# Kernel optimization log

Hardware: AMD Instinct MI355X
Metric: run time of the kernel (lower is better)

## Reference

```python
import jax, jax.numpy as jnp
import numpy as np


def setup_inputs() -> dict:
    key = jax.random.key(0)
    ks = jax.random.split(key, 16)
    B, S, L2 = 16, 1024, 2048

    def rn(k, shape, scale=0.1):
        return jax.random.normal(k, shape, dtype=jnp.float32) * scale

    return {
        "x": rn(ks[0], (B, S, 3), 1.0),
        "v1": rn(ks[1], (B, L2 + 1, 3), 1.0),
        "v2": rn(ks[2], (B, L2 + 1, 3), 1.0),
        # Attention: Linear(6, 1)
        "attn_w": rn(ks[3], (1, 6)),
        "attn_b": rn(ks[4], (1,)),
        # fc1: Linear(3, 16)
        "fc1_w": rn(ks[5], (16, 3)),
        "fc1_b": rn(ks[6], (16,)),
        # LSTM(16, 32, 1), gate order i,f,g,o -> 4*32 = 128
        "w_ih": rn(ks[7], (128, 16)),
        "w_hh": rn(ks[8], (128, 32)),
        "b_ih": rn(ks[9], (128,)),
        "b_hh": rn(ks[10], (128,)),
        # fc2: Linear(38, 16)
        "fc2_w": rn(ks[11], (16, 38)),
        "fc2_b": rn(ks[12], (16,)),
        # fc3: Linear(16, 3)
        "fc3_w": rn(ks[13], (3, 16)),
        "fc3_b": rn(ks[14], (3,)),
    }


def _attention(x, v, attn_w, attn_b):
    # Linear(6,1) over cat([x_i, key_j]) decomposes into x-part + key-part,
    # avoiding the original [B,S,L2,6] repeat/cat intermediate (same math).
    key_, value = v[:, :-1], v[:, 1:]          # [B,L2,3] each
    wx, wk = attn_w[0, :3], attn_w[0, 3:]
    scores = (x @ wx)[:, :, None] + (key_ @ wk)[:, None, :] + attn_b[0]  # [B,S,L2]
    a = jax.nn.softmax(scores, axis=-1)
    return jnp.einsum('bij,bjd->bid', a, value)  # [B,S,3]


def _lstm(x, w_ih, w_hh, b_ih, b_hh):
    # Single-layer batch_first LSTM, zero initial state, pytorch gate order i,f,g,o.
    B = x.shape[0]
    H = w_hh.shape[1]
    xg = x @ w_ih.T + (b_ih + b_hh)  # [B,S,4H] precomputed input contribution

    def step(carry, g_t):
        h, c = carry
        g = g_t + h @ w_hh.T
        i, f, gg, o = jnp.split(g, 4, axis=-1)
        c = jax.nn.sigmoid(f) * c + jax.nn.sigmoid(i) * jnp.tanh(gg)
        h = jax.nn.sigmoid(o) * jnp.tanh(c)
        return (h, c), h

    init = (jnp.zeros((B, H), x.dtype), jnp.zeros((B, H), x.dtype))
    _, hs = jax.lax.scan(step, init, jnp.swapaxes(xg, 0, 1))  # [S,B,H]
    return jnp.swapaxes(hs, 0, 1)  # [B,S,H]


def reference(x, v1, v2, attn_w, attn_b, fc1_w, fc1_b,
              w_ih, w_hh, b_ih, b_hh, fc2_w, fc2_b, fc3_w, fc3_b):
    a1 = _attention(x, v1, attn_w, attn_b)   # [B,S,3]
    a2 = _attention(x, v2, attn_w, attn_b)   # [B,S,3]
    h = _lstm(x @ fc1_w.T + fc1_b, w_ih, w_hh, b_ih, b_hh)  # [B,S,32]
    cat = jnp.concatenate([a1, a2, h], axis=-1)              # [B,S,38]
    out = jax.nn.relu(cat @ fc2_w.T + fc2_b) @ fc3_w.T + fc3_b
    return out  # [B,S,3]
```

## Files before the change

### kernel.cpp

```cpp
#include <hip/hip_runtime.h>
#include <hip/hip_bf16.h>

#define B_ 16
#define S_ 1024
#define L_ 2048
#define H_ 32

static __device__ __forceinline__ float sigm(float v) {
    return __builtin_amdgcn_rcpf(1.0f + __expf(-v));
}

static __device__ __forceinline__ float block_red_max(float v, float* buf, int tid) {
#pragma unroll
    for (int o = 32; o; o >>= 1) v = fmaxf(v, __shfl_down(v, o));
    if ((tid & 63) == 0) buf[tid >> 6] = v;
    __syncthreads();
    v = fmaxf(fmaxf(buf[0], buf[1]), fmaxf(buf[2], buf[3]));
    __syncthreads();
    return v;
}
static __device__ __forceinline__ float block_red_sum(float v, float* buf, int tid) {
#pragma unroll
    for (int o = 32; o; o >>= 1) v += __shfl_down(v, o);
    if ((tid & 63) == 0) buf[tid >> 6] = v;
    __syncthreads();
    v = buf[0] + buf[1] + buf[2] + buf[3];
    __syncthreads();
    return v;
}

__global__ __launch_bounds__(256) void attn_kernel(
    const float* __restrict__ v1, const float* __restrict__ v2,
    const float* __restrict__ attn_w, float* __restrict__ A)
{
    const int b   = blockIdx.x & 15;
    const int sel = blockIdx.x >> 4;
    const float* v = (sel ? v2 : v1) + (size_t)b * ((L_ + 1) * 3);
    const float wk0 = attn_w[3], wk1 = attn_w[4], wk2 = attn_w[5];
    const int tid = threadIdx.x;
    __shared__ float buf[4];

    float s[8];
    float mx = -3.4e38f;
#pragma unroll
    for (int k = 0; k < 8; ++k) {
        int jj = tid + (k << 8);
        const float* p = v + jj * 3;
        float sc = fmaf(p[2], wk2, fmaf(p[1], wk1, p[0] * wk0));
        s[k] = sc;
        mx = fmaxf(mx, sc);
    }
    mx = block_red_max(mx, buf, tid);

    float den = 0.f, a0 = 0.f, a1 = 0.f, a2 = 0.f;
#pragma unroll
    for (int k = 0; k < 8; ++k) {
        int jj = tid + (k << 8);
        float e = __expf(s[k] - mx);
        den += e;
        const float* p = v + (jj + 1) * 3;
        a0 = fmaf(e, p[0], a0);
        a1 = fmaf(e, p[1], a1);
        a2 = fmaf(e, p[2], a2);
    }
    den = block_red_sum(den, buf, tid);
    a0  = block_red_sum(a0,  buf, tid);
    a1  = block_red_sum(a1,  buf, tid);
    a2  = block_red_sum(a2,  buf, tid);
    if (tid == 0) {
        float inv = 1.0f / den;
        float* dst = A + sel * 48 + b * 3;
        dst[0] = a0 * inv; dst[1] = a1 * inv; dst[2] = a2 * inv;
    }
}

__global__ __launch_bounds__(64) void lstm_kernel(
    const float* __restrict__ x,
    const float* __restrict__ fc1_w,
    const float* __restrict__ fc1_b,
    const float* __restrict__ w_ih,
    const float* __restrict__ w_hh,
    const float* __restrict__ b_ih,
    const float* __restrict__ b_hh,
    float* __restrict__ h_out)
{
    const int b  = blockIdx.x;
    const int l  = threadIdx.x;
    const int j  = l & 31;
    const int hi = l >> 5;
    const int r0 = hi ? (32 + j) : j;
    const int r1 = hi ? (96 + j) : (64 + j);

    __shared__ float lds_x[S_ * 3];
    __shared__ float lds_h[64];

    {
        const float4* src = (const float4*)(x + (size_t)b * (S_ * 3));
        float4* dst = (float4*)lds_x;
#pragma unroll
        for (int m = 0; m < 12; ++m) dst[l + 64 * m] = src[l + 64 * m];
    }
    if (l < 32) lds_h[l] = 0.f;

    float wh0[H_], wh1[H_];
    {
        const float4* p0 = (const float4*)(w_hh + r0 * H_);
        const float4* p1 = (const float4*)(w_hh + r1 * H_);
#pragma unroll
        for (int m = 0; m < 8; ++m) {
            float4 a = p0[m];
            wh0[4*m] = a.x; wh0[4*m+1] = a.y; wh0[4*m+2] = a.z; wh0[4*m+3] = a.w;
            float4 c2 = p1[m];
            wh1[4*m] = c2.x; wh1[4*m+1] = c2.y; wh1[4*m+2] = c2.z; wh1[4*m+3] = c2.w;
        }
    }
    float W00 = 0, W01 = 0, W02 = 0, W10 = 0, W11 = 0, W12 = 0, bb0, bb1;
    {
        float s0 = 0, s1 = 0;
#pragma unroll
        for (int k = 0; k < 16; ++k) {
            float wi0 = w_ih[r0 * 16 + k], wi1 = w_ih[r1 * 16 + k];
            float f0 = fc1_w[k * 3 + 0], f1 = fc1_w[k * 3 + 1], f2 = fc1_w[k * 3 + 2];
            float fb = fc1_b[k];
            W00 = fmaf(wi0, f0, W00); W01 = fmaf(wi0, f1, W01); W02 = fmaf(wi0, f2, W02);
            s0  = fmaf(wi0, fb, s0);
            W10 = fmaf(wi1, f0, W10); W11 = fmaf(wi1, f1, W11); W12 = fmaf(wi1, f2, W12);
            s1  = fmaf(wi1, fb, s1);
        }
        bb0 = s0 + b_ih[r0] + b_hh[r0];
        bb1 = s1 + b_ih[r1] + b_hh[r1];
    }
    const float m1 = hi ? 1.0f : 2.0f;
    float c = 0.f;
    float* hob = h_out + ((size_t)b << 15);
    __syncthreads();

    for (int t = 0; t < S_; ++t) {
        const int rb = (t & 1) << 5;
        const int wb = rb ^ 32;
        float x0 = lds_x[3 * t], x1 = lds_x[3 * t + 1], x2 = lds_x[3 * t + 2];
        float a0 = fmaf(W02, x2, fmaf(W01, x1, fmaf(W00, x0, bb0)));
        float a1 = fmaf(W12, x2, fmaf(W11, x1, fmaf(W10, x0, bb1)));
#pragma unroll
        for (int m = 0; m < 8; ++m) {
            float4 hv = *(const float4*)&lds_h[rb + 4 * m];
            a0 = fmaf(wh0[4*m+0], hv.x, a0); a1 = fmaf(wh1[4*m+0], hv.x, a1);
            a0 = fmaf(wh0[4*m+1], hv.y, a0); a1 = fmaf(wh1[4*m+1], hv.y, a1);
            a0 = fmaf(wh0[4*m+2], hv.z, a0); a1 = fmaf(wh1[4*m+2], hv.z, a1);
            a0 = fmaf(wh0[4*m+3], hv.w, a0); a1 = fmaf(wh1[4*m+3], hv.w, a1);
        }
        float s0 = sigm(a0);
        float s1 = sigm(a1 * m1);
        float t0 = __shfl_xor(s0, 32);
        float t1 = __shfl_xor(s1, 32);
        float si = hi ? t0 : s0;
        float sf = hi ? s0 : t0;
        float sg = hi ? t1 : s1;
        float so = hi ? s1 : t1;
        float tg = fmaf(2.f, sg, -1.f);
        c = fmaf(sf, c, si * tg);
        float tc = fmaf(2.f, sigm(2.f * c), -1.f);
        float hval = so * tc;
        if (!hi) {
            lds_h[wb + j] = hval;
            hob[(t << 5) + j] = hval;
        }
        __syncthreads();
    }
}

__global__ __launch_bounds__(256) void final_kernel(
    const float* __restrict__ h,
    const float* __restrict__ A,
    const float* __restrict__ fc2_w,
    const float* __restrict__ fc2_b,
    const float* __restrict__ fc3_w,
    const float* __restrict__ fc3_b,
    float* __restrict__ out)
{
    __shared__ float sw2[16 * 38], sb2[16], sw3[48], sb3[3], sA[96];
    const int tid = threadIdx.x;
    for (int i = tid; i < 16 * 38; i += 256) sw2[i] = fc2_w[i];
    if (tid < 96) sA[tid] = A[tid];
    if (tid < 16) sb2[tid] = fc2_b[tid];
    if (tid < 48) sw3[tid] = fc3_w[tid];
    if (tid < 3)  sb3[tid] = fc3_b[tid];
    __syncthreads();

    const int p = blockIdx.x * 256 + tid;
    if (p >= B_ * S_) return;
    const int b = p >> 10;

    float hv[32];
    {
        const float4* hp = (const float4*)(h + ((size_t)p << 5));
#pragma unroll
        for (int m = 0; m < 8; ++m) {
            float4 t = hp[m];
            hv[4*m] = t.x; hv[4*m+1] = t.y; hv[4*m+2] = t.z; hv[4*m+3] = t.w;
        }
    }
    const float a10 = sA[b*3+0], a11 = sA[b*3+1], a12 = sA[b*3+2];
    const float a20 = sA[48+b*3+0], a21 = sA[48+b*3+1], a22 = sA[48+b*3+2];

    float y[16];
#pragma unroll
    for (int u = 0; u < 16; ++u) {
        const float* w = sw2 + u * 38;
        float acc = sb2[u];
        acc = fmaf(w[0], a10, acc); acc = fmaf(w[1], a11, acc); acc = fmaf(w[2], a12, acc);
        acc = fmaf(w[3], a20, acc); acc = fmaf(w[4], a21, acc); acc = fmaf(w[5], a22, acc);
#pragma unroll
        for (int k = 0; k < 32; ++k) acc = fmaf(w[6 + k], hv[k], acc);
        y[u] = fmaxf(acc, 0.f);
    }
#pragma unroll
    for (int d = 0; d < 3; ++d) {
        float o = sb3[d];
#pragma unroll
        for (int u = 0; u < 16; ++u) o = fmaf(sw3[d * 16 + u], y[u], o);
        out[p * 3 + d] = o;
    }
}

extern "C" void kernel_launch(void* const* d_in, const int* in_sizes, int n_in,
                              void* d_out, int out_size, void* d_ws, size_t ws_size,
                              hipStream_t stream) {
    const float* x      = (const float*)d_in[0];
    const float* v1     = (const float*)d_in[1];
    const float* v2     = (const float*)d_in[2];
    const float* attn_w = (const float*)d_in[3];
    const float* fc1_w  = (const float*)d_in[5];
    const float* fc1_b  = (const float*)d_in[6];
    const float* w_ih   = (const float*)d_in[7];
    const float* w_hh   = (const float*)d_in[8];
    const float* b_ih   = (const float*)d_in[9];
    const float* b_hh   = (const float*)d_in[10];
    const float* fc2_w  = (const float*)d_in[11];
    const float* fc2_b  = (const float*)d_in[12];
    const float* fc3_w  = (const float*)d_in[13];
    const float* fc3_b  = (const float*)d_in[14];
    float* out = (float*)d_out;

    float* Aws = (float*)d_ws;
    float* hws = (float*)((char*)d_ws + 4096);

    attn_kernel <<<32, 256, 0, stream>>>(v1, v2, attn_w, Aws);
    lstm_kernel <<<16, 64, 0, stream>>>(x, fc1_w, fc1_b, w_ih, w_hh, b_ih, b_hh, hws);
    final_kernel<<<64, 256, 0, stream>>>(hws, Aws, fc2_w, fc2_b, fc3_w, fc3_b, out);
}
```

Before: 432.7 us.

## Fuse attention into LSTM launch and streamline recurrent step without barriers

Merges the attention reduction into the LSTM kernel as 32 extra single-wave blocks using only wave shuffles, dropping one kernel launch. In the recurrent loop it removes the per-step __syncthreads, relying on the 64-thread block being a single wave64. It also splits the h vector dot product into two packed-FMA accumulator chains and uses exp2 with prescaled constants. Finally it unrolls by two with fixed double-buffer offsets and gives the global h store to the upper half-wave. The aim is a shorter serial latency per timestep. The cost is that correctness now depends on in-order LDS access within one wave, with no explicit barrier.

```diff
diff --git a/kernel.cpp b/kernel.cpp
--- a/kernel.cpp
+++ b/kernel.cpp
@@ -6,86 +6,76 @@
 #define L_ 2048
 #define H_ 32
 
-static __device__ __forceinline__ float sigm(float v) {
-    return __builtin_amdgcn_rcpf(1.0f + __expf(-v));
-}
-
-static __device__ __forceinline__ float block_red_max(float v, float* buf, int tid) {
-#pragma unroll
-    for (int o = 32; o; o >>= 1) v = fmaxf(v, __shfl_down(v, o));
-    if ((tid & 63) == 0) buf[tid >> 6] = v;
-    __syncthreads();
-    v = fmaxf(fmaxf(buf[0], buf[1]), fmaxf(buf[2], buf[3]));
-    __syncthreads();
-    return v;
-}
-static __device__ __forceinline__ float block_red_sum(float v, float* buf, int tid) {
-#pragma unroll
-    for (int o = 32; o; o >>= 1) v += __shfl_down(v, o);
-    if ((tid & 63) == 0) buf[tid >> 6] = v;
-    __syncthreads();
-    v = buf[0] + buf[1] + buf[2] + buf[3];
-    __syncthreads();
-    return v;
-}
-
-__global__ __launch_bounds__(256) void attn_kernel(
-    const float* __restrict__ v1, const float* __restrict__ v2,
-    const float* __restrict__ attn_w, float* __restrict__ A)
-{
-    const int b   = blockIdx.x & 15;
-    const int sel = blockIdx.x >> 4;
-    const float* v = (sel ? v2 : v1) + (size_t)b * ((L_ + 1) * 3);
-    const float wk0 = attn_w[3], wk1 = attn_w[4], wk2 = attn_w[5];
-    const int tid = threadIdx.x;
-    __shared__ float buf[4];
-
-    float s[8];
-    float mx = -3.4e38f;
-#pragma unroll
-    for (int k = 0; k < 8; ++k) {
-        int jj = tid + (k << 8);
-        const float* p = v + jj * 3;
-        float sc = fmaf(p[2], wk2, fmaf(p[1], wk1, p[0] * wk0));
-        s[k] = sc;
-        mx = fmaxf(mx, sc);
-    }
-    mx = block_red_max(mx, buf, tid);
-
-    float den = 0.f, a0 = 0.f, a1 = 0.f, a2 = 0.f;
-#pragma unroll
-    for (int k = 0; k < 8; ++k) {
-        int jj = tid + (k << 8);
-        float e = __expf(s[k] - mx);
-        den += e;
-        const float* p = v + (jj + 1) * 3;
-        a0 = fmaf(e, p[0], a0);
-        a1 = fmaf(e, p[1], a1);
-        a2 = fmaf(e, p[2], a2);
-    }
-    den = block_red_sum(den, buf, tid);
-    a0  = block_red_sum(a0,  buf, tid);
-    a1  = block_red_sum(a1,  buf, tid);
-    a2  = block_red_sum(a2,  buf, tid);
-    if (tid == 0) {
-        float inv = 1.0f / den;
-        float* dst = A + sel * 48 + b * 3;
-        dst[0] = a0 * inv; dst[1] = a1 * inv; dst[2] = a2 * inv;
-    }
-}
-
-__global__ __launch_bounds__(64) void lstm_kernel(
+typedef float f2v __attribute__((ext_vector_type(2)));
+typedef float f4v __attribute__((ext_vector_type(4)));
+
+static __device__ __forceinline__ f2v pkfma(f2v a, f2v b, f2v c) {
+    f2v d;
+    asm("v_pk_fma_f32 %0, %1, %2, %3" : "=v"(d) : "v"(a), "v"(b), "v"(c));
+    return d;
+}
+static __device__ __forceinline__ f2v pkadd(f2v a, f2v b) {
+    f2v d;
+    asm("v_pk_add_f32 %0, %1, %2" : "=v"(d) : "v"(a), "v"(b));
+    return d;
+}
+
+__global__ __launch_bounds__(64) void fused_attn_lstm(
     const float* __restrict__ x,
+    const float* __restrict__ v1,
+    const float* __restrict__ v2,
+    const float* __restrict__ attn_w,
     const float* __restrict__ fc1_w,
     const float* __restrict__ fc1_b,
     const float* __restrict__ w_ih,
     const float* __restrict__ w_hh,
     const float* __restrict__ b_ih,
     const float* __restrict__ b_hh,
+    float* __restrict__ A,
     float* __restrict__ h_out)
 {
-    const int b  = blockIdx.x;
-    const int l  = threadIdx.x;
+    const int blk = blockIdx.x;
+    const int l   = threadIdx.x;
+
+    if (blk >= 16) {
+        const int idx = blk - 16;
+        const int b = idx & 15, sel = idx >> 4;
+        const float* v = (sel ? v2 : v1) + (size_t)b * ((L_ + 1) * 3);
+        const float wk0 = attn_w[3], wk1 = attn_w[4], wk2 = attn_w[5];
+
+        float s[32];
+        float mx = -3.4e38f;
+#pragma unroll
+        for (int k = 0; k < 32; ++k) {
+            const float* p = v + (l + (k << 6)) * 3;
+            float sc = fmaf(p[2], wk2, fmaf(p[1], wk1, p[0] * wk0));
+            s[k] = sc; mx = fmaxf(mx, sc);
+        }
+#pragma unroll
+        for (int o = 1; o < 64; o <<= 1) mx = fmaxf(mx, __shfl_xor(mx, o));
+
+        float den = 0.f, a0 = 0.f, a1 = 0.f, a2 = 0.f;
+#pragma unroll
+        for (int k = 0; k < 32; ++k) {
+            float e = __expf(s[k] - mx);
+            const float* p = v + (l + (k << 6) + 1) * 3;
+            den += e;
+            a0 = fmaf(e, p[0], a0); a1 = fmaf(e, p[1], a1); a2 = fmaf(e, p[2], a2);
+        }
+#pragma unroll
+        for (int o = 1; o < 64; o <<= 1) {
+            den += __shfl_xor(den, o); a0 += __shfl_xor(a0, o);
+            a1  += __shfl_xor(a1, o);  a2 += __shfl_xor(a2, o);
+        }
+        if (l == 0) {
+            float inv = 1.0f / den;
+            float* dst = A + sel * 48 + b * 3;
+            dst[0] = a0 * inv; dst[1] = a1 * inv; dst[2] = a2 * inv;
+        }
+        return;
+    }
+
+    const int b  = blk;
     const int j  = l & 31;
     const int hi = l >> 5;
     const int r0 = hi ? (32 + j) : j;
@@ -95,25 +85,28 @@
     __shared__ float lds_h[64];
 
     {
-        const float4* src = (const float4*)(x + (size_t)b * (S_ * 3));
-        float4* dst = (float4*)lds_x;
+        const f4v* src = (const f4v*)(x + (size_t)b * (S_ * 3));
+        f4v* dst = (f4v*)lds_x;
 #pragma unroll
         for (int m = 0; m < 12; ++m) dst[l + 64 * m] = src[l + 64 * m];
     }
     if (l < 32) lds_h[l] = 0.f;
 
-    float wh0[H_], wh1[H_];
-    {
-        const float4* p0 = (const float4*)(w_hh + r0 * H_);
-        const float4* p1 = (const float4*)(w_hh + r1 * H_);
+    f2v wh0[16], wh1[16];
+    {
+        const f4v* p0 = (const f4v*)(w_hh + r0 * H_);
+        const f4v* p1 = (const f4v*)(w_hh + r1 * H_);
 #pragma unroll
         for (int m = 0; m < 8; ++m) {
-            float4 a = p0[m];
-            wh0[4*m] = a.x; wh0[4*m+1] = a.y; wh0[4*m+2] = a.z; wh0[4*m+3] = a.w;
-            float4 c2 = p1[m];
-            wh1[4*m] = c2.x; wh1[4*m+1] = c2.y; wh1[4*m+2] = c2.z; wh1[4*m+3] = c2.w;
-        }
-    }
+            f4v a = p0[m];
+            wh0[2*m]   = __builtin_shufflevector(a, a, 0, 1);
+            wh0[2*m+1] = __builtin_shufflevector(a, a, 2, 3);
+            f4v c2 = p1[m];
+            wh1[2*m]   = __builtin_shufflevector(c2, c2, 0, 1);
+            wh1[2*m+1] = __builtin_shufflevector(c2, c2, 2, 3);
+        }
+    }
+
     float W00 = 0, W01 = 0, W02 = 0, W10 = 0, W11 = 0, W12 = 0, bb0, bb1;
     {
         float s0 = 0, s1 = 0;
@@ -130,43 +123,53 @@
         bb0 = s0 + b_ih[r0] + b_hh[r0];
         bb1 = s1 + b_ih[r1] + b_hh[r1];
     }
-    const float m1 = hi ? 1.0f : 2.0f;
+
+    const float CE = -1.44269504f;
+    const float c1 = hi ? CE : 2.f * CE;
     float c = 0.f;
     float* hob = h_out + ((size_t)b << 15);
-    __syncthreads();
-
-    for (int t = 0; t < S_; ++t) {
-        const int rb = (t & 1) << 5;
-        const int wb = rb ^ 32;
-        float x0 = lds_x[3 * t], x1 = lds_x[3 * t + 1], x2 = lds_x[3 * t + 2];
-        float a0 = fmaf(W02, x2, fmaf(W01, x1, fmaf(W00, x0, bb0)));
-        float a1 = fmaf(W12, x2, fmaf(W11, x1, fmaf(W10, x0, bb1)));
-#pragma unroll
-        for (int m = 0; m < 8; ++m) {
-            float4 hv = *(const float4*)&lds_h[rb + 4 * m];
-            a0 = fmaf(wh0[4*m+0], hv.x, a0); a1 = fmaf(wh1[4*m+0], hv.x, a1);
-            a0 = fmaf(wh0[4*m+1], hv.y, a0); a1 = fmaf(wh1[4*m+1], hv.y, a1);
-            a0 = fmaf(wh0[4*m+2], hv.z, a0); a1 = fmaf(wh1[4*m+2], hv.z, a1);
-            a0 = fmaf(wh0[4*m+3], hv.w, a0); a1 = fmaf(wh1[4*m+3], hv.w, a1);
-        }
-        float s0 = sigm(a0);
-        float s1 = sigm(a1 * m1);
-        float t0 = __shfl_xor(s0, 32);
-        float t1 = __shfl_xor(s1, 32);
-        float si = hi ? t0 : s0;
-        float sf = hi ? s0 : t0;
-        float sg = hi ? t1 : s1;
-        float so = hi ? s1 : t1;
-        float tg = fmaf(2.f, sg, -1.f);
-        c = fmaf(sf, c, si * tg);
-        float tc = fmaf(2.f, sigm(2.f * c), -1.f);
-        float hval = so * tc;
-        if (!hi) {
-            lds_h[wb + j] = hval;
-            hob[(t << 5) + j] = hval;
-        }
-        __syncthreads();
-    }
+
+#define STEP(T, RB, WB) do {                                                          \
+        float x0 = lds_x[3*(T)], x1 = lds_x[3*(T)+1], x2 = lds_x[3*(T)+2];            \
+        f2v acc0a = { fmaf(W02,x2, fmaf(W01,x1, fmaf(W00,x0, bb0))), 0.f };           \
+        f2v acc1a = { fmaf(W12,x2, fmaf(W11,x1, fmaf(W10,x0, bb1))), 0.f };           \
+        f2v acc0b = { 0.f, 0.f };                                                     \
+        f2v acc1b = { 0.f, 0.f };                                                     \
+        _Pragma("unroll")                                                             \
+        for (int m = 0; m < 8; ++m) {                                                 \
+            f4v hv = *(const f4v*)&lds_h[(RB) + 4*m];                                 \
+            f2v hlo = __builtin_shufflevector(hv, hv, 0, 1);                          \
+            f2v hhi = __builtin_shufflevector(hv, hv, 2, 3);                          \
+            acc0a = pkfma(wh0[2*m],   hlo, acc0a);                                    \
+            acc1a = pkfma(wh1[2*m],   hlo, acc1a);                                    \
+            acc0b = pkfma(wh0[2*m+1], hhi, acc0b);                                    \
+            acc1b = pkfma(wh1[2*m+1], hhi, acc1b);                                    \
+        }                                                                             \
+        f2v acc0 = pkadd(acc0a, acc0b);                                               \
+        f2v acc1 = pkadd(acc1a, acc1b);                                               \
+        float a0 = acc0.x + acc0.y;                                                   \
+        float a1 = acc1.x + acc1.y;                                                   \
+        float s0 = __builtin_amdgcn_rcpf(1.f + __builtin_amdgcn_exp2f(a0 * CE));      \
+        float s1 = __builtin_amdgcn_rcpf(1.f + __builtin_amdgcn_exp2f(a1 * c1));      \
+        float t0 = __shfl_xor(s0, 32);                                                \
+        float t1 = __shfl_xor(s1, 32);                                                \
+        float si = hi ? t0 : s0;                                                      \
+        float sf = hi ? s0 : t0;                                                      \
+        float sg = hi ? t1 : s1;                                                      \
+        float so = hi ? s1 : t1;                                                      \
+        float tg = fmaf(2.f, sg, -1.f);                                               \
+        c = fmaf(sf, c, si * tg);                                                     \
+        float tc = fmaf(2.f, __builtin_amdgcn_rcpf(1.f + __builtin_amdgcn_exp2f(c * (2.f*CE))), -1.f); \
+        float hval = so * tc;                                                         \
+        if (!hi) lds_h[(WB) + j] = hval;                                              \
+        else     hob[((T) << 5) + j] = hval;                                          \
+    } while (0)
+
+    for (int t = 0; t < S_; t += 2) {
+        STEP(t,     0, 32);
+        STEP(t + 1, 32, 0);
+    }
+#undef STEP
 }
 
 __global__ __launch_bounds__(256) void final_kernel(
@@ -245,7 +248,7 @@
     float* Aws = (float*)d_ws;
     float* hws = (float*)((char*)d_ws + 4096);
 
-    attn_kernel <<<32, 256, 0, stream>>>(v1, v2, attn_w, Aws);
-    lstm_kernel <<<16, 64, 0, stream>>>(x, fc1_w, fc1_b, w_ih, w_hh, b_ih, b_hh, hws);
-    final_kernel<<<64, 256, 0, stream>>>(hws, Aws, fc2_w, fc2_b, fc3_w, fc3_b, out);
-}
+    fused_attn_lstm<<<48, 64, 0, stream>>>(x, v1, v2, attn_w, fc1_w, fc1_b,
+                                           w_ih, w_hh, b_ih, b_hh, Aws, hws);
+    final_kernel  <<<64, 256, 0, stream>>>(hws, Aws, fc2_w, fc2_b, fc3_w, fc3_b, out);
+}
```

New measurement: 395.8 us. 8.5% less time.
